# Performance work log

Hardware: AMD Instinct MI355X
Metric: run time of the kernel (lower is better)

## Reference

```python
import jax, jax.numpy as jnp
import numpy as np


def _squash(s):
    # s: [B, 10, 16]; norms reduce over the capsule-class dim (axis=1), as in torch code
    s_l2 = jnp.linalg.norm(s, axis=1)[:, :, None]   # [B, 16, 1]
    s_l1 = jnp.sum(jnp.abs(s), axis=1)[:, :, None]  # [B, 16, 1]
    return s_l2 / (1.0 + s_l2) * (jnp.swapaxes(s, 1, 2) / s_l1)  # [B, 16, 10]


def setup_inputs() -> dict:
    key = jax.random.key(0)
    ks = jax.random.split(key, 8)
    B = 1024
    x = jax.random.normal(ks[0], (B, 1, 28, 28), dtype=jnp.float32)
    conv1_w = jax.random.normal(ks[1], (256, 1, 9, 9), dtype=jnp.float32) * 0.05
    conv1_b = jnp.zeros((256,), dtype=jnp.float32)
    prim_w = jax.random.normal(ks[2], (32, 32, 1, 9, 9), dtype=jnp.float32) * 0.05
    prim_b = jnp.zeros((32,), dtype=jnp.float32)
    a = float(np.sqrt(6.0 / (8 + 16)))  # xavier-uniform bound for dig_W
    dig_W = jax.random.uniform(ks[3], (1152, 8, 16), jnp.float32, -a, a)
    dig_Wb = jnp.zeros((1152, 16), dtype=jnp.float32)
    out_w = jax.random.normal(ks[4], (10, 10, 16, 1), dtype=jnp.float32) * 0.05
    out_b = jnp.zeros((10,), dtype=jnp.float32)
    return dict(x=x, conv1_w=conv1_w, conv1_b=conv1_b, prim_w=prim_w, prim_b=prim_b,
                dig_W=dig_W, dig_Wb=dig_Wb, out_w=out_w, out_b=out_b)


def reference(x, conv1_w, conv1_b, prim_w, prim_b, dig_W, dig_Wb, out_w, out_b):
    # conv1: [B,1,28,28] -> [B,256,20,20]
    out = jax.lax.conv_general_dilated(
        x, conv1_w, window_strides=(1, 1), padding='VALID',
        dimension_numbers=('NCHW', 'OIHW', 'NCHW')) + conv1_b[None, :, None, None]
    out = jax.nn.relu(out)
    B = out.shape[0]
    out1 = out.reshape(B, 32, 8, 20, 20)
    # prim_layer Conv3d(32,32,[1,9,9],stride=[1,2,2]): -> [B,32,8,6,6]
    out1 = jax.lax.conv_general_dilated(
        out1, prim_w, window_strides=(1, 2, 2), padding='VALID',
        dimension_numbers=('NCDHW', 'OIDHW', 'NCDHW')) + prim_b[None, :, None, None, None]
    out1 = jax.nn.relu(out1)
    out1 = jnp.swapaxes(out1, 2, 4)        # [B,32,6,6,8]
    out1 = out1.reshape(B, 1152, 8)        # primary capsules
    # per-capsule affine: [B,1152,8] x [1152,8,16] -> [B,1152,16]
    u = jnp.einsum('bne,nef->bnf', out1, dig_W) + dig_Wb
    # dynamic routing, 3 iterations
    b = jnp.zeros((B, 10, 1152), dtype=u.dtype)
    v = None
    for _ in range(3):
        c = jax.nn.softmax(b, axis=1)                       # softmax over 10 classes
        s = jnp.einsum('bjn,bnf->bjf', c, u)                # [B,10,16]
        v = _squash(s)                                      # [B,16,10]
        b = b + jnp.swapaxes(jnp.matmul(u, v), 1, 2)        # [B,10,1152]
    # output conv2d(10,10,[16,1]) on [B,10,16,1] == einsum over (class-in, pose)
    logits = jnp.einsum('bif,oif->bo', jnp.swapaxes(v, 1, 2), out_w[..., 0]) + out_b
    return jax.nn.softmax(logits, axis=1)
```

## Files before the change

### kernel.cpp

```cpp
#include <hip/hip_runtime.h>
#include <math.h>

typedef __attribute__((ext_vector_type(8))) short bf16x8;
typedef __attribute__((ext_vector_type(4))) float f32x4;
#define MFMA16(a, b, c) __builtin_amdgcn_mfma_f32_16x16x32_bf16(a, b, c, 0, 0, 0)

union U8 { bf16x8 v; int i4[4]; };
union P4 { unsigned short h[4]; uint2 u2; };

__device__ __forceinline__ unsigned short f2bf(float x) {
    unsigned u = __builtin_bit_cast(unsigned, x);
    unsigned r = (u + 0x7fffu + ((u >> 16) & 1u)) >> 16;
    return (unsigned short)r;
}

__device__ __forceinline__ int koff_of(int kidx) {
    int grp = kidx >> 3, e = kidx & 7;
    if (grp < 9)  return grp * 9 + e;
    if (grp == 9) return e * 9 + 8;
    if (grp == 10) return (e == 0) ? 80 : -1;
    return -1;
}

#define CAPS_BYTES 37748736
#define A1F_ELEMS  24576
#define W3F_ELEMS  82944

#define SWZ(A) ((A) ^ ((((A) >> 7) & 7) << 4))

__global__ void k_prep(const float* __restrict__ c1w,
                       const float* __restrict__ pw,
                       unsigned short* __restrict__ w1f,
                       unsigned short* __restrict__ w3f)
{
    int idx = blockIdx.x * 256 + threadIdx.x;
    if (idx < A1F_ELEMS) {
        int e = idx & 7, lane = (idx >> 3) & 63, f = idx >> 9;
        int k3 = f % 3, m = (f / 3) & 1, d = f / 6;
        int ch = (lane & 15) + m * 16;
        int kidx = k3 * 32 + ((lane >> 4) << 3) + e;
        int ko = koff_of(kidx);
        w1f[idx] = f2bf(ko >= 0 ? c1w[(ch * 8 + d) * 81 + ko] : 0.f);
    } else if (idx < A1F_ELEMS + W3F_ELEMS) {
        int j = idx - A1F_ELEMS;
        int e = j & 7, lane = (j >> 3) & 63, f = j >> 9;
        int m = f & 1, tap = f >> 1;
        int oc = (lane & 15) + m * 16;
        int i = ((lane >> 4) << 3) + e;
        w3f[j] = f2bf(pw[oc * 2592 + i * 81 + tap]);
    }
}

#define ICS 40

__global__ __launch_bounds__(256, 4) void k_conv(
    const float* __restrict__ x,
    const float* __restrict__ c1b,
    const float* __restrict__ pb,
    const unsigned short* __restrict__ w1f,
    const unsigned short* __restrict__ w3f,
    float* __restrict__ caps)
{
    __shared__ __align__(16) unsigned short img[800];
    __shared__ __align__(16) unsigned short imgs[800];
    __shared__ __align__(128) unsigned short interm[400 * ICS];

    const int t = threadIdx.x;
    const int lane = t & 63, w = t >> 6;
    const int g = lane >> 4, col = lane & 15;
    const int b = blockIdx.x >> 3, d = blockIdx.x & 7;

    for (int idx = t; idx < 784; idx += 256) {
        unsigned short v = f2bf(x[b * 784 + idx]);
        img[idx] = v;
        if (idx > 0) imgs[idx - 1] = v;
    }
    __syncthreads();

    {
        bf16x8 a1[2][3];
        const bf16x8* w1p = (const bf16x8*)w1f;
#pragma unroll
        for (int m = 0; m < 2; ++m)
#pragma unroll
            for (int k3 = 0; k3 < 3; ++k3)
                a1[m][k3] = w1p[((d * 2 + m) * 3 + k3) * 64 + lane];

        float bias[2][4];
#pragma unroll
        for (int m = 0; m < 2; ++m)
#pragma unroll
            for (int r = 0; r < 4; ++r)
                bias[m][r] = c1b[(m * 16 + g * 4 + r) * 8 + d];

        for (int q = w; q < 25; q += 4) {
            int p = q * 16 + col;
            int py = p / 20, px = p - py * 20;
            int base = py * 28 + px;
            const unsigned short* rbase = (base & 1) ? &imgs[base - 1] : &img[base];

            bf16x8 bfrag[3];
#pragma unroll
            for (int k3 = 0; k3 < 2; ++k3) {
                int grp = k3 * 4 + g;
                U8 u8;
#pragma unroll
                for (int qq = 0; qq < 4; ++qq)
                    u8.i4[qq] = *(const int*)(rbase + grp * 28 + 2 * qq);
                bfrag[k3] = u8.v;
            }
            {
                U8 u8;
                if (g == 0) {
#pragma unroll
                    for (int qq = 0; qq < 4; ++qq)
                        u8.i4[qq] = *(const int*)(rbase + 8 * 28 + 2 * qq);
                } else if (g == 1) {
#pragma unroll
                    for (int e = 0; e < 8; ++e)
                        u8.v[e] = (short)img[base + e * 28 + 8];
                } else if (g == 2) {
                    u8.i4[0] = u8.i4[1] = u8.i4[2] = u8.i4[3] = 0;
                    u8.v[0] = (short)img[base + 8 * 28 + 8];
                } else {
                    u8.i4[0] = u8.i4[1] = u8.i4[2] = u8.i4[3] = 0;
                }
                bfrag[2] = u8.v;
            }

            f32x4 acc0 = {0.f, 0.f, 0.f, 0.f};
            f32x4 acc1 = {0.f, 0.f, 0.f, 0.f};
#pragma unroll
            for (int k3 = 0; k3 < 3; ++k3) {
                acc0 = MFMA16(a1[0][k3], bfrag[k3], acc0);
                acc1 = MFMA16(a1[1][k3], bfrag[k3], acc1);
            }
            P4 pk0, pk1;
#pragma unroll
            for (int r = 0; r < 4; ++r) {
                pk0.h[r] = f2bf(fmaxf(acc0[r] + bias[0][r], 0.f));
                pk1.h[r] = f2bf(fmaxf(acc1[r] + bias[1][r], 0.f));
            }
            int A0 = p * 80 + g * 8;
            int A1 = A0 + 32;
            *(uint2*)((char*)interm + SWZ(A0)) = pk0.u2;
            *(uint2*)((char*)interm + SWZ(A1)) = pk1.u2;
        }
    }
    __syncthreads();

    f32x4 acc[2][3];
#pragma unroll
    for (int m = 0; m < 2; ++m)
#pragma unroll
        for (int nt = 0; nt < 3; ++nt)
            acc[m][nt] = (f32x4){0.f, 0.f, 0.f, 0.f};
    {
        int abase[3];
#pragma unroll
        for (int nt = 0; nt < 3; ++nt) {
            int p2 = nt * 16 + col;
            int xw = p2 / 6, yh = p2 - xw * 6;
            int pos0 = (p2 < 36) ? (yh * 40 + xw * 2) : 0;
            abase[nt] = pos0 * 80 + g * 16;
        }
        const bf16x8* w3p = (const bf16x8*)w3f;
        int ky = 0, kx = w;
        for (int tap = w; tap < 81; tap += 4) {
            bf16x8 a0 = w3p[(tap * 2 + 0) * 64 + lane];
            bf16x8 a1v = w3p[(tap * 2 + 1) * 64 + lane];
            int koff80 = (ky * 20 + kx) * 80;
#pragma unroll
            for (int nt = 0; nt < 3; ++nt) {
                int A = abase[nt] + koff80;
                bf16x8 bfrag = *(const bf16x8*)((const char*)interm + SWZ(A));
                acc[0][nt] = MFMA16(a0, bfrag, acc[0][nt]);
                acc[1][nt] = MFMA16(a1v, bfrag, acc[1][nt]);
            }
            kx += 4;
            if (kx >= 9) { kx -= 9; ++ky; }
        }
    }
    __syncthreads();
    f32x4* rp = (f32x4*)&interm[0];
    {
#pragma unroll
        for (int m = 0; m < 2; ++m)
#pragma unroll
            for (int nt = 0; nt < 3; ++nt)
                rp[(w * 6 + m * 3 + nt) * 64 + lane] = acc[m][nt];
    }
    __syncthreads();
    for (int idx = t; idx < 384; idx += 256) {
        int tile = idx >> 6, ls = idx & 63;
        f32x4 s = rp[tile * 64 + ls];
#pragma unroll
        for (int ww = 1; ww < 4; ++ww)
            s += rp[(ww * 6 + tile) * 64 + ls];
        int m = tile / 3, nt = tile - m * 3;
        int p2 = nt * 16 + (ls & 15);
        if (p2 < 36) {
            int gr = ls >> 4;
#pragma unroll
            for (int r = 0; r < 4; ++r) {
                int oc = m * 16 + gr * 4 + r;
                caps[(b * 8 + d) * 1152 + oc * 36 + p2] = fmaxf(s[r] + pb[oc], 0.f);
            }
        }
    }
}

#define USB 1160
#define CSB 1160

__global__ __launch_bounds__(576, 5) void k_route(
    const float* __restrict__ caps,
    const float* __restrict__ W,
    const float* __restrict__ Wb,
    const float* __restrict__ ow,
    const float* __restrict__ ob,
    float* __restrict__ out)
{
    __shared__ __align__(16) unsigned short u_bf[16 * USB];
    __shared__ __align__(16) unsigned short c_bf[10 * CSB];
    __shared__ __align__(16) float sred[9 * 256];
    __shared__ __align__(16) float vv[16 * 12];
    __shared__ float ss[160];
    __shared__ float red2[16];

    const int t = threadIdx.x;
    const int lane = t & 63, wv = t >> 6;
    const int g = lane >> 4, col = lane & 15;
    const int b = blockIdx.x;
    const int n0 = 2 * t;

    {
        const int nl = t >> 2, fq = t & 3;
        for (int base = 0; base < 1152; base += 144) {
            int n = base + nl;
            float cv[8];
#pragma unroll
            for (int e = 0; e < 8; ++e) cv[e] = caps[(b * 8 + e) * 1152 + n];
            float4 a4 = ((const float4*)(Wb + n * 16))[fq];
#pragma unroll
            for (int e = 0; e < 8; ++e) {
                float4 w4 = ((const float4*)(W + n * 128 + e * 16))[fq];
                a4.x += cv[e] * w4.x; a4.y += cv[e] * w4.y;
                a4.z += cv[e] * w4.z; a4.w += cv[e] * w4.w;
            }
            u_bf[(fq * 4 + 0) * USB + n] = f2bf(a4.x);
            u_bf[(fq * 4 + 1) * USB + n] = f2bf(a4.y);
            u_bf[(fq * 4 + 2) * USB + n] = f2bf(a4.z);
            u_bf[(fq * 4 + 3) * USB + n] = f2bf(a4.w);
        }
    }
    float breg[2][10];
#pragma unroll
    for (int s = 0; s < 2; ++s)
#pragma unroll
        for (int jj = 0; jj < 10; ++jj) breg[s][jj] = 0.f;
    __syncthreads();

    const int jrow = (col < 10) ? col : 9;

    for (int iter = 0; iter < 3; ++iter) {
        {
            float cv2[2][10];
#pragma unroll
            for (int s = 0; s < 2; ++s) {
                float m = breg[s][0];
#pragma unroll
                for (int jj = 1; jj < 10; ++jj) m = fmaxf(m, breg[s][jj]);
                float sum = 0.f;
#pragma unroll
                for (int jj = 0; jj < 10; ++jj) { cv2[s][jj] = __expf(breg[s][jj] - m); sum += cv2[s][jj]; }
                float inv = 1.f / sum;
#pragma unroll
                for (int jj = 0; jj < 10; ++jj) cv2[s][jj] *= inv;
            }
#pragma unroll
            for (int jj = 0; jj < 10; ++jj) {
                unsigned pk = (unsigned)f2bf(cv2[0][jj]) | ((unsigned)f2bf(cv2[1][jj]) << 16);
                *(unsigned*)(&c_bf[jj * CSB + n0]) = pk;
            }
        }
        __syncthreads();
        {
            f32x4 sp = {0.f, 0.f, 0.f, 0.f};
#pragma unroll
            for (int mf = 0; mf < 4; ++mf) {
                int nk = wv * 128 + mf * 32 + g * 8;
                bf16x8 af = *(const bf16x8*)(&c_bf[jrow * CSB + nk]);
                bf16x8 bf = *(const bf16x8*)(&u_bf[col * USB + nk]);
                sp = MFMA16(af, bf, sp);
            }
            *(f32x4*)(&sred[wv * 256 + lane * 4]) = sp;
        }
        __syncthreads();
        if (t < 160) {
            int j = t >> 4, f = t & 15;
            int li = ((j >> 2) * 16 + f) * 4 + (j & 3);
            float s = 0.f;
#pragma unroll
            for (int ww = 0; ww < 9; ++ww) s += sred[ww * 256 + li];
            ss[j * 16 + f] = s;
        }
        __syncthreads();
        if (t < 16) {
            float sv[10], l2 = 0.f, l1 = 0.f;
#pragma unroll
            for (int jj = 0; jj < 10; ++jj) {
                sv[jj] = ss[jj * 16 + t];
                l2 += sv[jj] * sv[jj]; l1 += fabsf(sv[jj]);
            }
            l2 = sqrtf(l2);
            float scale = l2 / (1.f + l2) / l1;
#pragma unroll
            for (int jj = 0; jj < 10; ++jj) vv[t * 12 + jj] = sv[jj] * scale;
        }
        __syncthreads();
        if (iter < 2) {
#pragma unroll
            for (int f = 0; f < 16; ++f) {
                unsigned pair = *(const unsigned*)(&u_bf[f * USB + n0]);
                float ux = __builtin_bit_cast(float, pair << 16);
                float uy = __builtin_bit_cast(float, pair & 0xffff0000u);
                f32x4 v0 = *(const f32x4*)(&vv[f * 12]);
                f32x4 v1 = *(const f32x4*)(&vv[f * 12 + 4]);
                float2 v2 = *(const float2*)(&vv[f * 12 + 8]);
                breg[0][0] += ux * v0.x; breg[1][0] += uy * v0.x;
                breg[0][1] += ux * v0.y; breg[1][1] += uy * v0.y;
                breg[0][2] += ux * v0.z; breg[1][2] += uy * v0.z;
                breg[0][3] += ux * v0.w; breg[1][3] += uy * v0.w;
                breg[0][4] += ux * v1.x; breg[1][4] += uy * v1.x;
                breg[0][5] += ux * v1.y; breg[1][5] += uy * v1.y;
                breg[0][6] += ux * v1.z; breg[1][6] += uy * v1.z;
                breg[0][7] += ux * v1.w; breg[1][7] += uy * v1.w;
                breg[0][8] += ux * v2.x; breg[1][8] += uy * v2.x;
                breg[0][9] += ux * v2.y; breg[1][9] += uy * v2.y;
            }
        }
        __syncthreads();
    }

    if (t < 10) {
        float l = ob[t];
#pragma unroll
        for (int i2 = 0; i2 < 10; ++i2)
#pragma unroll
            for (int ff = 0; ff < 16; ++ff)
                l += vv[ff * 12 + i2] * ow[t * 160 + i2 * 16 + ff];
        red2[t] = l;
    }
    __syncthreads();
    if (t == 0) {
        float m = -1e30f;
        for (int o = 0; o < 10; ++o) m = fmaxf(m, red2[o]);
        float sum = 0.f; float e[10];
        for (int o = 0; o < 10; ++o) { e[o] = __expf(red2[o] - m); sum += e[o]; }
        float inv = 1.f / sum;
        for (int o = 0; o < 10; ++o) out[b * 10 + o] = e[o] * inv;
    }
}

extern "C" void kernel_launch(void* const* d_in, const int* in_sizes, int n_in,
                              void* d_out, int out_size, void* d_ws, size_t ws_size,
                              hipStream_t stream) {
    const float* x     = (const float*)d_in[0];
    const float* c1w   = (const float*)d_in[1];
    const float* c1b   = (const float*)d_in[2];
    const float* pw    = (const float*)d_in[3];
    const float* pb    = (const float*)d_in[4];
    const float* digW  = (const float*)d_in[5];
    const float* digWb = (const float*)d_in[6];
    const float* outw  = (const float*)d_in[7];
    const float* outb  = (const float*)d_in[8];
    float* out = (float*)d_out;

    float* caps = (float*)d_ws;
    unsigned short* w1f = (unsigned short*)((char*)d_ws + CAPS_BYTES);
    unsigned short* w3f = w1f + A1F_ELEMS;

    k_prep<<<dim3(420), dim3(256), 0, stream>>>(c1w, pw, w1f, w3f);
    k_conv<<<dim3(8192), dim3(256), 0, stream>>>(x, c1b, pb, w1f, w3f, caps);
    k_route<<<dim3(1024), dim3(576), 0, stream>>>(caps, digW, digWb, outw, outb, out);
}
```

Measured before the change: 187.7 us.

## Process two samples per routing block, drop LDS swizzle, restructure prim-conv tap loop

The routing kernel now handles two batch samples per 1024-thread block, splitting threads across both samples' capsules plus an extra partial set, which halves the block count and spreads fixed per-block overhead. The conv kernel drops the XOR swizzle on the intermediate LDS buffer, uses a hardware packed bf16 conversion instruction, and replaces the strided tap loop with per-wave kernel rows fully unrolled over kx. Risks include LDS bank conflicts without the swizzle, uneven tap work across waves, and higher LDS and register use in the routing kernel lowering occupancy.

Result: slower. 283.3 us (+51.0%).

```diff
diff --git a/kernel.cpp b/kernel.cpp
--- a/kernel.cpp
+++ b/kernel.cpp
@@ -6,12 +6,16 @@
 #define MFMA16(a, b, c) __builtin_amdgcn_mfma_f32_16x16x32_bf16(a, b, c, 0, 0, 0)
 
 union U8 { bf16x8 v; int i4[4]; };
-union P4 { unsigned short h[4]; uint2 u2; };
 
 __device__ __forceinline__ unsigned short f2bf(float x) {
     unsigned u = __builtin_bit_cast(unsigned, x);
     unsigned r = (u + 0x7fffu + ((u >> 16) & 1u)) >> 16;
     return (unsigned short)r;
+}
+__device__ __forceinline__ unsigned cvtpk(float lo, float hi) {
+    unsigned r;
+    asm("v_cvt_pk_bf16_f32 %0, %1, %2" : "=v"(r) : "v"(lo), "v"(hi));
+    return r;
 }
 
 __device__ __forceinline__ int koff_of(int kidx) {
@@ -25,8 +29,6 @@
 #define CAPS_BYTES 37748736
 #define A1F_ELEMS  24576
 #define W3F_ELEMS  82944
-
-#define SWZ(A) ((A) ^ ((((A) >> 7) & 7) << 4))
 
 __global__ void k_prep(const float* __restrict__ c1w,
                        const float* __restrict__ pw,
@@ -51,8 +53,6 @@
     }
 }
 
-#define ICS 40
-
 __global__ __launch_bounds__(256, 4) void k_conv(
     const float* __restrict__ x,
     const float* __restrict__ c1b,
@@ -63,7 +63,7 @@
 {
     __shared__ __align__(16) unsigned short img[800];
     __shared__ __align__(16) unsigned short imgs[800];
-    __shared__ __align__(128) unsigned short interm[400 * ICS];
+    __shared__ __align__(128) unsigned short interm[400 * 40];
 
     const int t = threadIdx.x;
     const int lane = t & 63, w = t >> 6;
@@ -135,16 +135,14 @@
                 acc0 = MFMA16(a1[0][k3], bfrag[k3], acc0);
                 acc1 = MFMA16(a1[1][k3], bfrag[k3], acc1);
             }
-            P4 pk0, pk1;
+            float r0[4], r1[4];
 #pragma unroll
             for (int r = 0; r < 4; ++r) {
-                pk0.h[r] = f2bf(fmaxf(acc0[r] + bias[0][r], 0.f));
-                pk1.h[r] = f2bf(fmaxf(acc1[r] + bias[1][r], 0.f));
-            }
-            int A0 = p * 80 + g * 8;
-            int A1 = A0 + 32;
-            *(uint2*)((char*)interm + SWZ(A0)) = pk0.u2;
-            *(uint2*)((char*)interm + SWZ(A1)) = pk1.u2;
+                r0[r] = fmaxf(acc0[r] + bias[0][r], 0.f);
+                r1[r] = fmaxf(acc1[r] + bias[1][r], 0.f);
+            }
+            *(uint2*)(&interm[p * 40 + g * 4])      = make_uint2(cvtpk(r0[0], r0[1]), cvtpk(r0[2], r0[3]));
+            *(uint2*)(&interm[p * 40 + 16 + g * 4]) = make_uint2(cvtpk(r1[0], r1[1]), cvtpk(r1[2], r1[3]));
         }
     }
     __syncthreads();
@@ -165,20 +163,51 @@
             abase[nt] = pos0 * 80 + g * 16;
         }
         const bf16x8* w3p = (const bf16x8*)w3f;
-        int ky = 0, kx = w;
-        for (int tap = w; tap < 81; tap += 4) {
-            bf16x8 a0 = w3p[(tap * 2 + 0) * 64 + lane];
-            bf16x8 a1v = w3p[(tap * 2 + 1) * 64 + lane];
-            int koff80 = (ky * 20 + kx) * 80;
-#pragma unroll
-            for (int nt = 0; nt < 3; ++nt) {
-                int A = abase[nt] + koff80;
-                bf16x8 bfrag = *(const bf16x8*)((const char*)interm + SWZ(A));
-                acc[0][nt] = MFMA16(a0, bfrag, acc[0][nt]);
-                acc[1][nt] = MFMA16(a1v, bfrag, acc[1][nt]);
-            }
-            kx += 4;
-            if (kx >= 9) { kx -= 9; ++ky; }
+        const char* ib = (const char*)interm;
+
+        for (int rr = 0; rr < 2; ++rr) {
+            const int ky = 2 * w + rr;
+            const bf16x8* wrow = w3p + (ky * 9) * 128;
+            const char* B0 = ib + abase[0] + ky * 1600;
+            const char* B1 = ib + abase[1] + ky * 1600;
+            const char* B2 = ib + abase[2] + ky * 1600;
+#pragma unroll
+            for (int kx = 0; kx < 9; ++kx) {
+                bf16x8 a0  = wrow[kx * 128 + lane];
+                bf16x8 a1v = wrow[kx * 128 + 64 + lane];
+                bf16x8 b0 = *(const bf16x8*)(B0 + kx * 80);
+                bf16x8 b1 = *(const bf16x8*)(B1 + kx * 80);
+                bf16x8 b2 = *(const bf16x8*)(B2 + kx * 80);
+                acc[0][0] = MFMA16(a0, b0, acc[0][0]);
+                acc[1][0] = MFMA16(a1v, b0, acc[1][0]);
+                acc[0][1] = MFMA16(a0, b1, acc[0][1]);
+                acc[1][1] = MFMA16(a1v, b1, acc[1][1]);
+                acc[0][2] = MFMA16(a0, b2, acc[0][2]);
+                acc[1][2] = MFMA16(a1v, b2, acc[1][2]);
+            }
+        }
+        {
+            const bf16x8* wrow = w3p + 72 * 128;
+            const char* B0 = ib + abase[0] + 12800;
+            const char* B1 = ib + abase[1] + 12800;
+            const char* B2 = ib + abase[2] + 12800;
+            int kx0 = 2 * w;
+            int nkx = (w == 3) ? 3 : 2;
+#pragma unroll 3
+            for (int q = 0; q < nkx; ++q) {
+                int kx = kx0 + q;
+                bf16x8 a0  = wrow[kx * 128 + lane];
+                bf16x8 a1v = wrow[kx * 128 + 64 + lane];
+                bf16x8 b0 = *(const bf16x8*)(B0 + kx * 80);
+                bf16x8 b1 = *(const bf16x8*)(B1 + kx * 80);
+                bf16x8 b2 = *(const bf16x8*)(B2 + kx * 80);
+                acc[0][0] = MFMA16(a0, b0, acc[0][0]);
+                acc[1][0] = MFMA16(a1v, b0, acc[1][0]);
+                acc[0][1] = MFMA16(a0, b1, acc[0][1]);
+                acc[1][1] = MFMA16(a1v, b1, acc[1][1]);
+                acc[0][2] = MFMA16(a0, b2, acc[0][2]);
+                acc[1][2] = MFMA16(a1v, b2, acc[1][2]);
+            }
         }
     }
     __syncthreads();
@@ -213,7 +242,7 @@
 #define USB 1160
 #define CSB 1160
 
-__global__ __launch_bounds__(576, 5) void k_route(
+__global__ __launch_bounds__(1024) void k_route(
     const float* __restrict__ caps,
     const float* __restrict__ W,
     const float* __restrict__ Wb,
@@ -221,26 +250,34 @@
     const float* __restrict__ ob,
     float* __restrict__ out)
 {
-    __shared__ __align__(16) unsigned short u_bf[16 * USB];
-    __shared__ __align__(16) unsigned short c_bf[10 * CSB];
-    __shared__ __align__(16) float sred[9 * 256];
-    __shared__ __align__(16) float vv[16 * 12];
-    __shared__ float ss[160];
-    __shared__ float red2[16];
+    __shared__ __align__(16) unsigned short u_bf[2 * 16 * USB];
+    __shared__ __align__(16) unsigned short c_bf[2 * 10 * CSB];
+    __shared__ __align__(16) float sred[18 * 256];
+    __shared__ __align__(16) float vv[2 * 192];
+    __shared__ float ss[2 * 160];
+    __shared__ float red2[32];
 
     const int t = threadIdx.x;
     const int lane = t & 63, wv = t >> 6;
     const int g = lane >> 4, col = lane & 15;
-    const int b = blockIdx.x;
-    const int n0 = 2 * t;
+    const int b0 = blockIdx.x * 2;
+
+    const int mbs = (t >= 576);
+    const int mn0 = 2 * t - mbs * 1152;
+    const bool xact = (t < 128);
+    const int xn0 = 896 + 2 * t;
 
     {
         const int nl = t >> 2, fq = t & 3;
-        for (int base = 0; base < 1152; base += 144) {
-            int n = base + nl;
+#pragma unroll
+        for (int it = 0; it < 9; ++it) {
+            int row = it * 256 + nl;
+            int bs = row >= 1152;
+            int n = row - bs * 1152;
+            const float* capb = caps + (size_t)(b0 + bs) * 9216;
             float cv[8];
 #pragma unroll
-            for (int e = 0; e < 8; ++e) cv[e] = caps[(b * 8 + e) * 1152 + n];
+            for (int e = 0; e < 8; ++e) cv[e] = capb[e * 1152 + n];
             float4 a4 = ((const float4*)(Wb + n * 16))[fq];
 #pragma unroll
             for (int e = 0; e < 8; ++e) {
@@ -248,21 +285,21 @@
                 a4.x += cv[e] * w4.x; a4.y += cv[e] * w4.y;
                 a4.z += cv[e] * w4.z; a4.w += cv[e] * w4.w;
             }
-            u_bf[(fq * 4 + 0) * USB + n] = f2bf(a4.x);
-            u_bf[(fq * 4 + 1) * USB + n] = f2bf(a4.y);
-            u_bf[(fq * 4 + 2) * USB + n] = f2bf(a4.z);
-            u_bf[(fq * 4 + 3) * USB + n] = f2bf(a4.w);
-        }
-    }
-    float breg[2][10];
+            unsigned short* ub = u_bf + (size_t)bs * 16 * USB;
+            ub[(fq * 4 + 0) * USB + n] = f2bf(a4.x);
+            ub[(fq * 4 + 1) * USB + n] = f2bf(a4.y);
+            ub[(fq * 4 + 2) * USB + n] = f2bf(a4.z);
+            ub[(fq * 4 + 3) * USB + n] = f2bf(a4.w);
+        }
+    }
+    float breg[2][10], xreg[2][10];
 #pragma unroll
     for (int s = 0; s < 2; ++s)
 #pragma unroll
-        for (int jj = 0; jj < 10; ++jj) breg[s][jj] = 0.f;
+        for (int jj = 0; jj < 10; ++jj) { breg[s][jj] = 0.f; xreg[s][jj] = 0.f; }
     __syncthreads();
 
     const int jrow = (col < 10) ? col : 9;
-
     for (int iter = 0; iter < 3; ++iter) {
         {
             float cv2[2][10];
@@ -278,88 +315,147 @@
 #pragma unroll
                 for (int jj = 0; jj < 10; ++jj) cv2[s][jj] *= inv;
             }
-#pragma unroll
-            for (int jj = 0; jj < 10; ++jj) {
-                unsigned pk = (unsigned)f2bf(cv2[0][jj]) | ((unsigned)f2bf(cv2[1][jj]) << 16);
-                *(unsigned*)(&c_bf[jj * CSB + n0]) = pk;
+            unsigned short* cb = c_bf + (size_t)mbs * 10 * CSB;
+#pragma unroll
+            for (int jj = 0; jj < 10; ++jj)
+                *(unsigned*)(&cb[jj * CSB + mn0]) = cvtpk(cv2[0][jj], cv2[1][jj]);
+            if (xact) {
+                float xv[2][10];
+#pragma unroll
+                for (int s = 0; s < 2; ++s) {
+                    float m = xreg[s][0];
+#pragma unroll
+                    for (int jj = 1; jj < 10; ++jj) m = fmaxf(m, xreg[s][jj]);
+                    float sum = 0.f;
+#pragma unroll
+                    for (int jj = 0; jj < 10; ++jj) { xv[s][jj] = __expf(xreg[s][jj] - m); sum += xv[s][jj]; }
+                    float inv = 1.f / sum;
+#pragma unroll
+                    for (int jj = 0; jj < 10; ++jj) xv[s][jj] *= inv;
+                }
+                unsigned short* cb1 = c_bf + (size_t)10 * CSB;
+#pragma unroll
+                for (int jj = 0; jj < 10; ++jj)
+                    *(unsigned*)(&cb1[jj * CSB + xn0]) = cvtpk(xv[0][jj], xv[1][jj]);
             }
         }
         __syncthreads();
         {
-            f32x4 sp = {0.f, 0.f, 0.f, 0.f};
-#pragma unroll
-            for (int mf = 0; mf < 4; ++mf) {
-                int nk = wv * 128 + mf * 32 + g * 8;
-                bf16x8 af = *(const bf16x8*)(&c_bf[jrow * CSB + nk]);
-                bf16x8 bf = *(const bf16x8*)(&u_bf[col * USB + nk]);
-                sp = MFMA16(af, bf, sp);
-            }
-            *(f32x4*)(&sred[wv * 256 + lane * 4]) = sp;
+            int c0 = wv;
+            {
+                int bs = c0 >= 9;
+                int nb = (c0 - bs * 9) * 128;
+                const unsigned short* cb = c_bf + (size_t)bs * 10 * CSB;
+                const unsigned short* ub = u_bf + (size_t)bs * 16 * USB;
+                f32x4 sp = {0.f, 0.f, 0.f, 0.f};
+#pragma unroll
+                for (int mf = 0; mf < 4; ++mf) {
+                    int nk = nb + mf * 32 + g * 8;
+                    bf16x8 af = *(const bf16x8*)(&cb[jrow * CSB + nk]);
+                    bf16x8 bf = *(const bf16x8*)(&ub[col * USB + nk]);
+                    sp = MFMA16(af, bf, sp);
+                }
+                *(f32x4*)(&sred[c0 * 256 + lane * 4]) = sp;
+            }
+            if (wv < 2) {
+                int c1 = 16 + wv;
+                int bs = 1;
+                int nb = (c1 - 9) * 128;
+                const unsigned short* cb = c_bf + (size_t)bs * 10 * CSB;
+                const unsigned short* ub = u_bf + (size_t)bs * 16 * USB;
+                f32x4 sp = {0.f, 0.f, 0.f, 0.f};
+#pragma unroll
+                for (int mf = 0; mf < 4; ++mf) {
+                    int nk = nb + mf * 32 + g * 8;
+                    bf16x8 af = *(const bf16x8*)(&cb[jrow * CSB + nk]);
+                    bf16x8 bf = *(const bf16x8*)(&ub[col * USB + nk]);
+                    sp = MFMA16(af, bf, sp);
+                }
+                *(f32x4*)(&sred[c1 * 256 + lane * 4]) = sp;
+            }
         }
         __syncthreads();
-        if (t < 160) {
-            int j = t >> 4, f = t & 15;
+        if (t < 320) {
+            int bs = t >= 160;
+            int r = t - bs * 160;
+            int j = r >> 4, f = r & 15;
             int li = ((j >> 2) * 16 + f) * 4 + (j & 3);
             float s = 0.f;
 #pragma unroll
-            for (int ww = 0; ww < 9; ++ww) s += sred[ww * 256 + li];
-            ss[j * 16 + f] = s;
+            for (int cc = 0; cc < 9; ++cc) s += sred[(bs * 9 + cc) * 256 + li];
+            ss[bs * 160 + j * 16 + f] = s;
         }
         __syncthreads();
-        if (t < 16) {
+        if (t < 32) {
+            int bs = t >= 16, f = t & 15;
             float sv[10], l2 = 0.f, l1 = 0.f;
 #pragma unroll
             for (int jj = 0; jj < 10; ++jj) {
-                sv[jj] = ss[jj * 16 + t];
+                sv[jj] = ss[bs * 160 + jj * 16 + f];
                 l2 += sv[jj] * sv[jj]; l1 += fabsf(sv[jj]);
             }
             l2 = sqrtf(l2);
             float scale = l2 / (1.f + l2) / l1;
 #pragma unroll
-            for (int jj = 0; jj < 10; ++jj) vv[t * 12 + jj] = sv[jj] * scale;
+            for (int jj = 0; jj < 10; ++jj) vv[bs * 192 + f * 12 + jj] = sv[jj] * scale;
         }
         __syncthreads();
         if (iter < 2) {
-#pragma unroll
-            for (int f = 0; f < 16; ++f) {
-                unsigned pair = *(const unsigned*)(&u_bf[f * USB + n0]);
-                float ux = __builtin_bit_cast(float, pair << 16);
-                float uy = __builtin_bit_cast(float, pair & 0xffff0000u);
-                f32x4 v0 = *(const f32x4*)(&vv[f * 12]);
-                f32x4 v1 = *(const f32x4*)(&vv[f * 12 + 4]);
-                float2 v2 = *(const float2*)(&vv[f * 12 + 8]);
-                breg[0][0] += ux * v0.x; breg[1][0] += uy * v0.x;
-                breg[0][1] += ux * v0.y; breg[1][1] += uy * v0.y;
-                breg[0][2] += ux * v0.z; breg[1][2] += uy * v0.z;
-                breg[0][3] += ux * v0.w; breg[1][3] += uy * v0.w;
-                breg[0][4] += ux * v1.x; breg[1][4] += uy * v1.x;
-                breg[0][5] += ux * v1.y; breg[1][5] += uy * v1.y;
-                breg[0][6] += ux * v1.z; breg[1][6] += uy * v1.z;
-                breg[0][7] += ux * v1.w; breg[1][7] += uy * v1.w;
-                breg[0][8] += ux * v2.x; breg[1][8] += uy * v2.x;
-                breg[0][9] += ux * v2.y; breg[1][9] += uy * v2.y;
+            {
+                const unsigned short* ub = u_bf + (size_t)mbs * 16 * USB;
+                const float* vb = vv + mbs * 192;
+#pragma unroll
+                for (int f = 0; f < 16; ++f) {
+                    unsigned pair = *(const unsigned*)(&ub[f * USB + mn0]);
+                    float ux = __builtin_bit_cast(float, pair << 16);
+                    float uy = __builtin_bit_cast(float, pair & 0xffff0000u);
+#pragma unroll
+                    for (int jj = 0; jj < 10; ++jj) {
+                        float vj = vb[f * 12 + jj];
+                        breg[0][jj] += ux * vj;
+                        breg[1][jj] += uy * vj;
+                    }
+                }
+            }
+            if (xact) {
+                const unsigned short* ub = u_bf + (size_t)16 * USB;
+                const float* vb = vv + 192;
+#pragma unroll
+                for (int f = 0; f < 16; ++f) {
+                    unsigned pair = *(const unsigned*)(&ub[f * USB + xn0]);
+                    float ux = __builtin_bit_cast(float, pair << 16);
+                    float uy = __builtin_bit_cast(float, pair & 0xffff0000u);
+#pragma unroll
+                    for (int jj = 0; jj < 10; ++jj) {
+                        float vj = vb[f * 12 + jj];
+                        xreg[0][jj] += ux * vj;
+                        xreg[1][jj] += uy * vj;
+                    }
+                }
             }
         }
         __syncthreads();
     }
 
-    if (t < 10) {
-        float l = ob[t];
+    if (t < 20) {
+        int bs = t >= 10, o = t - bs * 10;
+        const float* vb = vv + bs * 192;
+        float l = ob[o];
 #pragma unroll
         for (int i2 = 0; i2 < 10; ++i2)
 #pragma unroll
             for (int ff = 0; ff < 16; ++ff)
-                l += vv[ff * 12 + i2] * ow[t * 160 + i2 * 16 + ff];
-        red2[t] = l;
-    }
-    __syncthreads();
-    if (t == 0) {
+                l += vb[ff * 12 + i2] * ow[o * 160 + i2 * 16 + ff];
+        red2[bs * 16 + o] = l;
+    }
+    __syncthreads();
+    if (t < 2) {
         float m = -1e30f;
-        for (int o = 0; o < 10; ++o) m = fmaxf(m, red2[o]);
+        for (int o = 0; o < 10; ++o) m = fmaxf(m, red2[t * 16 + o]);
         float sum = 0.f; float e[10];
-        for (int o = 0; o < 10; ++o) { e[o] = __expf(red2[o] - m); sum += e[o]; }
+        for (int o = 0; o < 10; ++o) { e[o] = __expf(red2[t * 16 + o] - m); sum += e[o]; }
         float inv = 1.f / sum;
-        for (int o = 0; o < 10; ++o) out[b * 10 + o] = e[o] * inv;
+        for (int o = 0; o < 10; ++o) out[(b0 + t) * 10 + o] = e[o] * inv;
     }
 }
 
@@ -383,5 +479,5 @@
 
     k_prep<<<dim3(420), dim3(256), 0, stream>>>(c1w, pw, w1f, w3f);
     k_conv<<<dim3(8192), dim3(256), 0, stream>>>(x, c1b, pb, w1f, w3f, caps);
-    k_route<<<dim3(1024), dim3(576), 0, stream>>>(caps, digW, digWb, outw, outb, out);
-}
+    k_route<<<dim3(512), dim3(1024), 0, stream>>>(caps, digW, digWb, outw, outb, out);
+}
```
